# Kernel tuning notes

Hardware: AMD Instinct MI355X
Metric: run time of the kernel (lower is better)

Reference implementation:

```python
import jax, jax.numpy as jnp
import numpy as np

B, L, E, H = 4, 4096, 1024, 16
D = E // H  # head_dim = 64
EPS = 1e-4


def setup_inputs() -> dict:
    key = jax.random.key(0)
    k1, k2, k3 = jax.random.split(key, 3)
    x = jax.random.normal(k1, (B, L, E), dtype=jnp.float32)
    W_qkv = jax.random.normal(k2, (E, 3 * E), dtype=jnp.float32) * (1.0 / np.sqrt(E))
    b_qkv = jnp.zeros((3 * E,), dtype=jnp.float32)
    W_out = jax.random.normal(k3, (E, E), dtype=jnp.float32) * (1.0 / np.sqrt(E))
    b_out = jnp.zeros((E,), dtype=jnp.float32)
    return {"x": x, "W_qkv": W_qkv, "b_qkv": b_qkv, "W_out": W_out, "b_out": b_out}


def reference(x, W_qkv, b_qkv, W_out, b_out):
    Bb, Ll, Ee = x.shape
    qkv = x @ W_qkv + b_qkv                      # [B, L, 3E]
    q, k, v = jnp.split(qkv, 3, axis=-1)
    # [B, H, L, D]
    q = q.reshape(Bb, Ll, H, D).transpose(0, 2, 1, 3)
    k = k.reshape(Bb, Ll, H, D).transpose(0, 2, 1, 3)
    v = v.reshape(Bb, Ll, H, D).transpose(0, 2, 1, 3)

    positions = jnp.arange(Ll, dtype=jnp.float32).reshape(1, 1, Ll, 1)
    cos_w = jnp.cos(jnp.pi / 2 * positions / Ll)
    sin_w = jnp.sin(jnp.pi / 2 * positions / Ll)

    q_prime = jax.nn.relu(q)
    k_prime = jax.nn.relu(k)

    q_cos, q_sin = q_prime * cos_w, q_prime * sin_w
    k_cos, k_sin = k_prime * cos_w, k_prime * sin_w

    # O(L) linear attention: accumulate KV outer products per head
    kv_cos = jnp.einsum('bhld,bhle->bhde', k_cos, v)      # [B,H,D,D]
    kv_sin = jnp.einsum('bhld,bhle->bhde', k_sin, v)
    context = (jnp.einsum('bhld,bhde->bhle', q_cos, kv_cos)
               + jnp.einsum('bhld,bhde->bhle', q_sin, kv_sin))  # [B,H,L,D]

    k_cos_sum = k_cos.sum(axis=2)                          # [B,H,D]
    k_sin_sum = k_sin.sum(axis=2)
    norm = (jnp.einsum('bhld,bhd->bhl', q_cos, k_cos_sum)
            + jnp.einsum('bhld,bhd->bhl', q_sin, k_sin_sum))

    output = context / (norm[..., None] + EPS)
    output = output.transpose(0, 2, 1, 3).reshape(Bb, Ll, Ee)
    return output @ W_out + b_out
```

## Files before the change

kernel.cpp:

```cpp
#include <hip/hip_runtime.h>
#include <hip/hip_bf16.h>
#include <cstdint>
#include <cstddef>

#define BB 4
#define LL 4096
#define HH 16
#define M1 16384
#define E3 3072
#define EE 1024
#define ANGC 3.8349519697141029e-4f
#define EPSC 1e-4f

typedef __attribute__((ext_vector_type(8))) short bf16x8;
typedef __attribute__((ext_vector_type(4))) float f32x4;
typedef __attribute__((ext_vector_type(8))) unsigned short us8;

static __device__ __forceinline__ float bf2f(unsigned short u) {
  union { unsigned int i; float f; } a; a.i = ((unsigned int)u) << 16; return a.f;
}
static __device__ __forceinline__ unsigned short f2bf(float x) {
  union { float f; unsigned int i; } a; a.f = x;
  unsigned int r = a.i + 0x7FFFu + ((a.i >> 16) & 1u);
  return (unsigned short)(r >> 16);
}
static __device__ __forceinline__ void gload16(const void* g, void* l) {
  __builtin_amdgcn_global_load_lds((const __attribute__((address_space(1))) void*)g,
                                   (__attribute__((address_space(3))) void*)l, 16, 0, 0);
}

#define BAR()   asm volatile("s_barrier" ::: "memory")
#define VMC4()  asm volatile("s_waitcnt vmcnt(4)" ::: "memory")
#define VMC0()  asm volatile("s_waitcnt vmcnt(0)" ::: "memory")
#define PRIO1() __builtin_amdgcn_s_setprio(1)
#define PRIO0() __builtin_amdgcn_s_setprio(0)

__global__ __launch_bounds__(256) void k_cvt_bf16(const float* __restrict__ src,
                                                  unsigned short* __restrict__ dst, int n8) {
  int i = blockIdx.x * 256 + threadIdx.x;
  if (i >= n8) return;
  const float4* s = (const float4*)src + (size_t)i * 2;
  float4 a = s[0], b = s[1];
  us8 o;
  o[0]=f2bf(a.x); o[1]=f2bf(a.y); o[2]=f2bf(a.z); o[3]=f2bf(a.w);
  o[4]=f2bf(b.x); o[5]=f2bf(b.y); o[6]=f2bf(b.z); o[7]=f2bf(b.w);
  *(us8*)(dst + (size_t)i * 8) = o;
}

__global__ __launch_bounds__(256) void k_transpose_bf16(const float* __restrict__ src,
                                                        unsigned short* __restrict__ dst,
                                                        int R, int C) {
  __shared__ float tile[32][33];
  int c0 = blockIdx.x * 32, r0 = blockIdx.y * 32;
  int tx = threadIdx.x & 31, ty = threadIdx.x >> 5;
#pragma unroll
  for (int k = 0; k < 4; ++k)
    tile[ty + 8*k][tx] = src[(size_t)(r0 + ty + 8*k) * C + c0 + tx];
  __syncthreads();
#pragma unroll
  for (int k = 0; k < 4; ++k)
    dst[(size_t)(c0 + ty + 8*k) * R + r0 + tx] = f2bf(tile[tx][ty + 8*k]);
}


static __device__ __forceinline__ bf16x8 rdfrag(const char* base, int row, int ck) {
  return *(const bf16x8*)(base + row * 128 + (((ck) ^ ((row) & 7)) << 4));
}

static __device__ __forceinline__ void stage2h(const unsigned short* __restrict__ base,
                                               size_t off, size_t rowK64, char* ldst) {
  gload16(base + off, ldst);
  gload16(base + off + rowK64, ldst + 8192);
}

#define PH_FIRST(AbP, BbP, AR)                                                  \
  do {                                                                          \
    _Pragma("unroll")                                                           \
    for (int n = 0; n < 4; ++n) {                                               \
      const int br = wc * 64 + n * 16 + lr;                                     \
      bF[n][0] = rdfrag((BbP), br, lg);                                         \
      bF[n][1] = rdfrag((BbP), br, 4 + lg);                                     \
    }                                                                           \
    AR[0][0] = rdfrag((AbP), wr * 128 + lr, lg);                                \
    AR[0][1] = rdfrag((AbP), wr * 128 + lr, 4 + lg);                            \
    AR[1][0] = rdfrag((AbP), wr * 128 + 16 + lr, lg);                           \
    AR[1][1] = rdfrag((AbP), wr * 128 + 16 + lr, 4 + lg);                       \
  } while (0)

#define PH_A(AbP, mb, AR)                                                       \
  do {                                                                          \
    AR[0][0] = rdfrag((AbP), wr * 128 + (mb) * 16 + lr, lg);                    \
    AR[0][1] = rdfrag((AbP), wr * 128 + (mb) * 16 + lr, 4 + lg);                \
    AR[1][0] = rdfrag((AbP), wr * 128 + (mb) * 16 + 16 + lr, lg);               \
    AR[1][1] = rdfrag((AbP), wr * 128 + (mb) * 16 + 16 + lr, 4 + lg);           \
  } while (0)

#define MMA16(mb, AR)                                                           \
  do {                                                                          \
    _Pragma("unroll")                                                           \
    for (int kk = 0; kk < 2; ++kk) {                                            \
      _Pragma("unroll")                                                         \
      for (int n = 0; n < 4; ++n) {                                             \
        acc[(mb)][n] = __builtin_amdgcn_mfma_f32_16x16x32_bf16(                 \
            AR[0][kk], bF[n][kk], acc[(mb)][n], 0, 0, 0);                       \
        acc[(mb) + 1][n] = __builtin_amdgcn_mfma_f32_16x16x32_bf16(             \
            AR[1][kk], bF[n][kk], acc[(mb) + 1][n], 0, 0, 0);                   \
      }                                                                         \
    }                                                                           \
  } while (0)

template<int MODE>
__global__ __launch_bounds__(512, 2) void k_gemm256(const unsigned short* __restrict__ A,
                                                    const unsigned short* __restrict__ Bt,
                                                    const float* __restrict__ bias,
                                                    void* __restrict__ Cout,
                                                    int N, int K) {
  __shared__ __align__(16) unsigned short lds[4][16384];
  const int tid = threadIdx.x;
  const int wid = tid >> 6, lane = tid & 63;
  const int lr = lane & 15, lg = lane >> 4;
  const int wr = wid >> 2, wc = wid & 3;

  const int nx = gridDim.x;
  const int rawbid = blockIdx.y * nx + blockIdx.x;
  const int xcd = rawbid & 7, s = rawbid >> 3;
  const int g = s >> 5, r = s & 31;
  const int bm = (xcd * 8 + (r & 7)) * 256;
  const int bn = (g * 4 + (r >> 3)) * 256;

  char* LA0 = (char*)&lds[0][0];
  char* LB0 = (char*)&lds[1][0];
  char* LA1 = (char*)&lds[2][0];
  char* LB1 = (char*)&lds[3][0];

  f32x4 acc[8][4] = {};
  bf16x8 bF[4][2], aF[2][2], aG[2][2];

  const int rr = tid >> 3, cc = tid & 7;
  const size_t rowK64 = (size_t)64 * K, rowK128 = (size_t)128 * K;
  const size_t aoff = (size_t)(bm + rr) * K + ((cc ^ (rr & 7)) << 3);
  const size_t boff = (size_t)(bn + rr) * K + ((cc ^ (rr & 7)) << 3);
  char* const dst16 = (char*)0 + tid * 16;

#define STAGE_A(h, kt, L) stage2h(A,  aoff + (h) * rowK128 + (kt), rowK64, (L) + (h) * 16384 + tid * 16)
#define STAGE_B(h, kt, L) stage2h(Bt, boff + (h) * rowK128 + (kt), rowK64, (L) + (h) * 16384 + tid * 16)

  const int NT = K >> 6, NI = NT >> 1;

  STAGE_A(0, 0, LA0); STAGE_A(1, 0, LA0);
  STAGE_B(0, 0, LB0); STAGE_B(1, 0, LB0);
  STAGE_B(0, 64, LB1); STAGE_B(1, 64, LB1);
  VMC4();
  BAR();

  for (int it = 0; it < NI; ++it) {
    const int kt1 = (2*it + 1) << 6;
    const int kt2 = (2*it + 2) << 6;
    const int kt3 = (2*it + 3) << 6;
    const bool s2 = kt2 < K, s3 = kt3 < K;

    PH_FIRST(LA0, LB0, aF);
    STAGE_A(0, kt1, LA1);
    BAR(); PRIO1(); MMA16(0, aF); PRIO0();

    PH_A(LA0, 2, aG);
    STAGE_A(1, kt1, LA1);
    BAR(); PRIO1(); MMA16(2, aG); PRIO0();

    PH_A(LA0, 4, aF);
    if (s2) STAGE_B(0, kt2, LB0);
    BAR(); PRIO1(); MMA16(4, aF); PRIO0();

    PH_A(LA0, 6, aG);
    if (s2) STAGE_B(1, kt2, LB0);
    BAR(); PRIO1(); MMA16(6, aG); PRIO0();
    if (it == NI - 1) { VMC0(); } else { VMC4(); }
    BAR();

    PH_FIRST(LA1, LB1, aF);
    if (s2) STAGE_A(0, kt2, LA0);
    BAR(); PRIO1(); MMA16(0, aF); PRIO0();

    PH_A(LA1, 2, aG);
    if (s2) STAGE_A(1, kt2, LA0);
    BAR(); PRIO1(); MMA16(2, aG); PRIO0();

    PH_A(LA1, 4, aF);
    if (s3) STAGE_B(0, kt3, LB1);
    BAR(); PRIO1(); MMA16(4, aF); PRIO0();

    PH_A(LA1, 6, aG);
    if (s3) STAGE_B(1, kt3, LB1);
    BAR(); PRIO1(); MMA16(6, aG); PRIO0();
    VMC4();
    BAR();
  }
#undef STAGE_A
#undef STAGE_B

  {
    float* strip = (float*)((char*)&lds[0][0] + wid * 16384);
    float bias_v[4]; bool relu_v[4];
#pragma unroll
    for (int n = 0; n < 4; ++n) {
      int col = bn + wc*64 + n*16 + lr;
      bias_v[n] = bias[col];
      relu_v[n] = (MODE == 0) && (col < 2048);
    }
#pragma unroll
    for (int m = 0; m < 8; ++m) {
#pragma unroll
      for (int n = 0; n < 4; ++n)
#pragma unroll
        for (int j = 0; j < 4; ++j) {
          float v = acc[m][n][j] + bias_v[n];
          if (relu_v[n]) v = fmaxf(v, 0.0f);
          strip[(lg*4 + j)*68 + n*16 + lr] = v;
        }
#pragma unroll
      for (int itr = 0; itr < 4; ++itr) {
        int ch = itr*64 + lane;
        int row = ch >> 4, cg = ch & 15;
        float4 v = *(const float4*)(strip + row*68 + cg*4);
        size_t base = (size_t)(bm + wr*128 + m*16 + row) * N + bn + wc*64 + cg*4;
        if (MODE == 0) {
          ushort4 o;
          o.x = f2bf(v.x); o.y = f2bf(v.y); o.z = f2bf(v.z); o.w = f2bf(v.w);
          *(ushort4*)((unsigned short*)Cout + base) = o;
        } else {
          *(float4*)((float*)Cout + base) = v;
        }
      }
    }
  }
  (void)dst16;
}

__global__ __launch_bounds__(256) void k_stage2(const unsigned short* __restrict__ qkv,
                                                float* __restrict__ kvb,
                                                float* __restrict__ ksumb) {
  __shared__ __align__(16) unsigned short kcT[4096];
  __shared__ __align__(16) unsigned short ksT[4096];
  __shared__ __align__(16) unsigned short vT [4096];
  const int tid = threadIdx.x;
  const int head = blockIdx.y;
  const int b = head >> 4, h = head & 15;
  const int lane = tid & 63, wid = tid >> 6;
  const int lr = lane & 15, lg = lane >> 4;
  const int mt = wid >> 1, eh = wid & 1;
  const int lp = tid & 31;
  const int piece = tid >> 5;

  f32x4 acc[2][4] = {};
  float ksacc = 0.0f;
  const int mtk = tid >> 6, dk = tid & 63;
  const size_t qbase = (size_t)b * LL * E3;

  for (int sc = 0; sc < 4; ++sc) {
    const int lbase = blockIdx.x * 256 + sc * 64;
    __syncthreads();
    {
      const int l0 = 2 * lp;
      const int p0 = lbase + l0;
      float s0, c0, s1, c1;
      __sincosf((float)p0 * ANGC, &s0, &c0);
      __sincosf((float)(p0 + 1) * ANGC, &s1, &c1);
      const unsigned short* kp = qkv + qbase + (size_t)p0 * E3 + 1024 + h*64 + piece*8;
      us8 kr0 = *(const us8*)kp;
      us8 kr1 = *(const us8*)(kp + E3);
      us8 vr0 = *(const us8*)(kp + 1024);
      us8 vr1 = *(const us8*)(kp + 1024 + E3);
#pragma unroll
      for (int i = 0; i < 8; ++i) {
        int d = piece*8 + i;
        float ka = bf2f(kr0[i]), kb = bf2f(kr1[i]);
        unsigned int kcp = (unsigned int)f2bf(c0*ka) | ((unsigned int)f2bf(c1*kb) << 16);
        unsigned int ksp = (unsigned int)f2bf(s0*ka) | ((unsigned int)f2bf(s1*kb) << 16);
        unsigned int vp  = (unsigned int)vr0[i] | ((unsigned int)vr1[i] << 16);
        int off = d*128 + ((((l0 >> 3) ^ (d & 7))) << 4) + (l0 & 7) * 2;
        *(unsigned int*)((char*)kcT + off) = kcp;
        *(unsigned int*)((char*)ksT + off) = ksp;
        *(unsigned int*)((char*)vT  + off) = vp;
      }
    }
    __syncthreads();
    if (tid < 128) {
      const unsigned short* basep = mtk ? ksT : kcT;
      float sum = 0.0f;
#pragma unroll
      for (int cch = 0; cch < 8; ++cch) {
        us8 r = *(const us8*)((const char*)basep + dk*128 + ((cch ^ (dk & 7)) << 4));
#pragma unroll
        for (int i = 0; i < 8; ++i) sum += bf2f(r[i]);
      }
      ksacc += sum;
    }
    {
      const unsigned short* kT = mt ? ksT : kcT;
      bf16x8 af[2][2], bf[2][4];
#pragma unroll
      for (int kk = 0; kk < 2; ++kk) {
#pragma unroll
        for (int m = 0; m < 2; ++m) {
          int e = eh*32 + m*16 + lr;
          af[kk][m] = *(const bf16x8*)((const char*)vT + e*128 + ((((kk*4)+lg) ^ (e & 7)) << 4));
        }
#pragma unroll
        for (int n = 0; n < 4; ++n) {
          int d = n*16 + lr;
          bf[kk][n] = *(const bf16x8*)((const char*)kT + d*128 + ((((kk*4)+lg) ^ (d & 7)) << 4));
        }
      }
#pragma unroll
      for (int kk = 0; kk < 2; ++kk)
#pragma unroll
        for (int m = 0; m < 2; ++m)
#pragma unroll
          for (int n = 0; n < 4; ++n)
            acc[m][n] = __builtin_amdgcn_mfma_f32_16x16x32_bf16(af[kk][m], bf[kk][n], acc[m][n], 0, 0, 0);
    }
  }
  float* dst = kvb + (size_t)head * 8192 + mt * 4096;
#pragma unroll
  for (int m = 0; m < 2; ++m)
#pragma unroll
    for (int n = 0; n < 4; ++n)
#pragma unroll
      for (int j = 0; j < 4; ++j) {
        int e = eh*32 + m*16 + lg*4 + j;
        int d = n*16 + lr;
        atomicAdd(&dst[e*64 + d], acc[m][n][j]);
      }
  if (tid < 128) atomicAdd(&ksumb[head*128 + mtk*64 + dk], ksacc);
}

__global__ __launch_bounds__(256) void k_stage3(const unsigned short* __restrict__ qkv,
                                                const float* __restrict__ kvb,
                                                const float* __restrict__ ksumb,
                                                unsigned short* __restrict__ att) {
  __shared__ __align__(16) unsigned short Bl[144 * 64];
  const int tid = threadIdx.x;
  const int head = blockIdx.y;
  const int b = head >> 4, h = head & 15;
  const int l0 = blockIdx.x * 128;
  const int lane = tid & 63, w = tid >> 6;
  const int lr = lane & 15, lg = lane >> 4;

  {
    int c = tid >> 1, half = tid & 1;
    const float* src = kvb + (size_t)head * 8192 + (c >> 6) * 4096 + (c & 63) * 64 + half * 32;
    float fv[32];
#pragma unroll
    for (int q = 0; q < 8; ++q) *(float4*)(fv + q*4) = *(const float4*)(src + q*4);
#pragma unroll
    for (int q2 = 0; q2 < 4; ++q2) {
      us8 o;
#pragma unroll
      for (int i = 0; i < 8; ++i) o[i] = f2bf(fv[q2*8 + i]);
      int chunk = half*4 + q2;
      *(us8*)((char*)Bl + c*128 + ((chunk ^ (c & 7)) << 4)) = o;
    }
    if (tid < 16) {
      int cc = 128 + (tid >> 3), q = tid & 7;
      const float* s2 = ksumb + head*128 + (tid >> 3)*64 + q*8;
      us8 o;
#pragma unroll
      for (int i = 0; i < 8; ++i) o[i] = f2bf(s2[i]);
      *(us8*)((char*)Bl + cc*128 + ((q ^ (cc & 7)) << 4)) = o;
    } else if (tid < 128) {
      int idx = tid - 16;
      int cc = 130 + (idx >> 3), q = idx & 7;
      us8 o = {0,0,0,0,0,0,0,0};
      *(us8*)((char*)Bl + cc*128 + ((q ^ (cc & 7)) << 4)) = o;
    }
  }
  __syncthreads();

  f32x4 acc[2][9] = {};
  bf16x8 af[2][2];
  const size_t qrow0 = (size_t)(b * LL + l0 + w * 32);
#pragma unroll
  for (int kk = 0; kk < 2; ++kk)
#pragma unroll
    for (int m = 0; m < 2; ++m)
      af[m][kk] = *(const bf16x8*)(qkv + (qrow0 + m*16 + lr) * E3 + h*64 + kk*32 + lg*8);
#pragma unroll
  for (int kk = 0; kk < 2; ++kk)
#pragma unroll
    for (int n = 0; n < 9; ++n) {
      int cc = n*16 + lr;
      bf16x8 bb = *(const bf16x8*)((const char*)Bl + cc*128 + ((((kk*4)+lg) ^ (cc & 7)) << 4));
#pragma unroll
      for (int m = 0; m < 2; ++m)
        acc[m][n] = __builtin_amdgcn_mfma_f32_16x16x32_bf16(af[m][kk], bb, acc[m][n], 0, 0, 0);
    }

  __syncthreads();
  unsigned short* strip = (unsigned short*)Bl + w * 2048;
#pragma unroll
  for (int m = 0; m < 2; ++m)
#pragma unroll
    for (int j = 0; j < 4; ++j) {
      int rloc = m*16 + lg*4 + j;
      int pos = l0 + w*32 + rloc;
      float s_, c_;
      __sincosf((float)pos * ANGC, &s_, &c_);
      float nc = __shfl(acc[m][8][j], lane & 48, 64);
      float ns = __shfl(acc[m][8][j], (lane & 48) | 1, 64);
      float rn = 1.0f / (c_ * nc + s_ * ns + EPSC);
#pragma unroll
      for (int n = 0; n < 4; ++n) {
        float ctx = (c_ * acc[m][n][j] + s_ * acc[m][n+4][j]) * rn;
        strip[rloc*64 + n*16 + lr] = f2bf(ctx);
      }
    }
  __syncthreads();
#pragma unroll
  for (int p = 0; p < 4; ++p) {
    int ch = p*64 + lane;
    int row = ch >> 3, piece = ch & 7;
    us8 o = *(const us8*)(strip + row*64 + piece*8);
    *(us8*)(att + (size_t)(b*LL + l0 + w*32 + row) * EE + h*64 + piece*8) = o;
  }
}

extern "C" void kernel_launch(void* const* d_in, const int* in_sizes, int n_in,
                              void* d_out, int out_size, void* d_ws, size_t ws_size,
                              hipStream_t stream) {
  const float* x     = (const float*)d_in[0];
  const float* W_qkv = (const float*)d_in[1];
  const float* b_qkv = (const float*)d_in[2];
  const float* W_out = (const float*)d_in[3];
  const float* b_out = (const float*)d_in[4];

  char* w = (char*)d_ws;
  unsigned short* xb  = (unsigned short*)(w);
  unsigned short* qkv = (unsigned short*)(w + 33554432);
  unsigned short* WqT = (unsigned short*)(w + 134217728);
  unsigned short* WoT = (unsigned short*)(w + 140509184);
  float* kvb   = (float*)(w + 142606336);
  float* ksum  = (float*)(w + 144703488);
  unsigned short* att = xb;

  hipMemsetAsync(kvb, 0, 2097152 + 32768, stream);
  k_cvt_bf16<<<8192, 256, 0, stream>>>(x, xb, 2097152);
  k_transpose_bf16<<<dim3(96, 32), 256, 0, stream>>>(W_qkv, WqT, 1024, 3072);
  k_transpose_bf16<<<dim3(32, 32), 256, 0, stream>>>(W_out, WoT, 1024, 1024);
  k_gemm256<0><<<dim3(12, 64), 512, 0, stream>>>(xb, WqT, b_qkv, (void*)qkv, 3072, 1024);
  k_stage2<<<dim3(16, 64), 256, 0, stream>>>(qkv, kvb, ksum);
  k_stage3<<<dim3(32, 64), 256, 0, stream>>>(qkv, kvb, ksum, att);
  k_gemm256<1><<<dim3(4, 64), 512, 0, stream>>>(att, WoT, b_out, d_out, 1024, 1024);
}
```

Before: 237.1 us.

## Switch GEMM to 32x32x16 MFMA tiles and fuse prep kernels into one launch

The GEMM inner loop moves from 16x16x32 bf16 MFMA fragments to 32x32x16 MFMA, changing the register fragment layout, the LDS read pattern and the epilogue row mapping. The aim is fewer LDS fragment reads per FLOP and denser matrix-core issue. Launch bounds drop from 2 to 1 blocks per CU, which gives more registers for the larger accumulators but lowers occupancy. The conversion and two weight-transpose kernels are merged into a single launch to cut launch overhead.

```diff
diff --git a/kernel.cpp b/kernel.cpp
--- a/kernel.cpp
+++ b/kernel.cpp
@@ -14,6 +14,7 @@
 
 typedef __attribute__((ext_vector_type(8))) short bf16x8;
 typedef __attribute__((ext_vector_type(4))) float f32x4;
+typedef __attribute__((ext_vector_type(16))) float f32x16;
 typedef __attribute__((ext_vector_type(8))) unsigned short us8;
 
 static __device__ __forceinline__ float bf2f(unsigned short u) {
@@ -35,23 +36,11 @@
 #define PRIO1() __builtin_amdgcn_s_setprio(1)
 #define PRIO0() __builtin_amdgcn_s_setprio(0)
 
-__global__ __launch_bounds__(256) void k_cvt_bf16(const float* __restrict__ src,
-                                                  unsigned short* __restrict__ dst, int n8) {
-  int i = blockIdx.x * 256 + threadIdx.x;
-  if (i >= n8) return;
-  const float4* s = (const float4*)src + (size_t)i * 2;
-  float4 a = s[0], b = s[1];
-  us8 o;
-  o[0]=f2bf(a.x); o[1]=f2bf(a.y); o[2]=f2bf(a.z); o[3]=f2bf(a.w);
-  o[4]=f2bf(b.x); o[5]=f2bf(b.y); o[6]=f2bf(b.z); o[7]=f2bf(b.w);
-  *(us8*)(dst + (size_t)i * 8) = o;
-}
-
-__global__ __launch_bounds__(256) void k_transpose_bf16(const float* __restrict__ src,
-                                                        unsigned short* __restrict__ dst,
-                                                        int R, int C) {
-  __shared__ float tile[32][33];
-  int c0 = blockIdx.x * 32, r0 = blockIdx.y * 32;
+static __device__ __forceinline__ void transpose_body(const float* __restrict__ src,
+                                                      unsigned short* __restrict__ dst,
+                                                      int R, int C, int bx, int by,
+                                                      float (*tile)[33]) {
+  int c0 = bx * 32, r0 = by * 32;
   int tx = threadIdx.x & 31, ty = threadIdx.x >> 5;
 #pragma unroll
   for (int k = 0; k < 4; ++k)
@@ -60,6 +49,31 @@
 #pragma unroll
   for (int k = 0; k < 4; ++k)
     dst[(size_t)(c0 + ty + 8*k) * R + r0 + tx] = f2bf(tile[tx][ty + 8*k]);
+}
+
+__global__ __launch_bounds__(256) void k_prep(const float* __restrict__ x,
+                                              const float* __restrict__ Wq,
+                                              const float* __restrict__ Wo,
+                                              unsigned short* __restrict__ xb,
+                                              unsigned short* __restrict__ WqT,
+                                              unsigned short* __restrict__ WoT) {
+  __shared__ float tile[32][33];
+  const int bid = blockIdx.x;
+  if (bid < 8192) {
+    int i = bid * 256 + threadIdx.x;
+    const float4* s = (const float4*)x + (size_t)i * 2;
+    float4 a = s[0], b = s[1];
+    us8 o;
+    o[0]=f2bf(a.x); o[1]=f2bf(a.y); o[2]=f2bf(a.z); o[3]=f2bf(a.w);
+    o[4]=f2bf(b.x); o[5]=f2bf(b.y); o[6]=f2bf(b.z); o[7]=f2bf(b.w);
+    *(us8*)(xb + (size_t)i * 8) = o;
+  } else if (bid < 8192 + 3072) {
+    int r = bid - 8192;
+    transpose_body(Wq, WqT, 1024, 3072, r % 96, r / 96, tile);
+  } else {
+    int r = bid - 11264;
+    transpose_body(Wo, WoT, 1024, 1024, r % 32, r / 32, tile);
+  }
 }
 
 
@@ -73,44 +87,35 @@
   gload16(base + off + rowK64, ldst + 8192);
 }
 
-#define PH_FIRST(AbP, BbP, AR)                                                  \
+#define PH_B(BbP)                                                               \
   do {                                                                          \
     _Pragma("unroll")                                                           \
-    for (int n = 0; n < 4; ++n) {                                               \
-      const int br = wc * 64 + n * 16 + lr;                                     \
-      bF[n][0] = rdfrag((BbP), br, lg);                                         \
-      bF[n][1] = rdfrag((BbP), br, 4 + lg);                                     \
-    }                                                                           \
-    AR[0][0] = rdfrag((AbP), wr * 128 + lr, lg);                                \
-    AR[0][1] = rdfrag((AbP), wr * 128 + lr, 4 + lg);                            \
-    AR[1][0] = rdfrag((AbP), wr * 128 + 16 + lr, lg);                           \
-    AR[1][1] = rdfrag((AbP), wr * 128 + 16 + lr, 4 + lg);                       \
+    for (int nb = 0; nb < 2; ++nb)                                              \
+      _Pragma("unroll")                                                         \
+      for (int kk = 0; kk < 4; ++kk)                                            \
+        bK[nb][kk] = rdfrag((BbP), wc * 64 + nb * 32 + l31, kk * 2 + l5);       \
   } while (0)
 
-#define PH_A(AbP, mb, AR)                                                       \
-  do {                                                                          \
-    AR[0][0] = rdfrag((AbP), wr * 128 + (mb) * 16 + lr, lg);                    \
-    AR[0][1] = rdfrag((AbP), wr * 128 + (mb) * 16 + lr, 4 + lg);                \
-    AR[1][0] = rdfrag((AbP), wr * 128 + (mb) * 16 + 16 + lr, lg);               \
-    AR[1][1] = rdfrag((AbP), wr * 128 + (mb) * 16 + 16 + lr, 4 + lg);           \
-  } while (0)
-
-#define MMA16(mb, AR)                                                           \
+#define PH_A32(AbP, mb, AR)                                                     \
   do {                                                                          \
     _Pragma("unroll")                                                           \
-    for (int kk = 0; kk < 2; ++kk) {                                            \
-      _Pragma("unroll")                                                         \
-      for (int n = 0; n < 4; ++n) {                                             \
-        acc[(mb)][n] = __builtin_amdgcn_mfma_f32_16x16x32_bf16(                 \
-            AR[0][kk], bF[n][kk], acc[(mb)][n], 0, 0, 0);                       \
-        acc[(mb) + 1][n] = __builtin_amdgcn_mfma_f32_16x16x32_bf16(             \
-            AR[1][kk], bF[n][kk], acc[(mb) + 1][n], 0, 0, 0);                   \
-      }                                                                         \
+    for (int kk = 0; kk < 4; ++kk)                                              \
+      AR[kk] = rdfrag((AbP), wr * 128 + (mb) * 32 + l31, kk * 2 + l5);          \
+  } while (0)
+
+#define MMA8(mb, AR)                                                            \
+  do {                                                                          \
+    _Pragma("unroll")                                                           \
+    for (int kk = 0; kk < 4; ++kk) {                                            \
+      acc[(mb)][0] = __builtin_amdgcn_mfma_f32_32x32x16_bf16(                   \
+          AR[kk], bK[0][kk], acc[(mb)][0], 0, 0, 0);                            \
+      acc[(mb)][1] = __builtin_amdgcn_mfma_f32_32x32x16_bf16(                   \
+          AR[kk], bK[1][kk], acc[(mb)][1], 0, 0, 0);                            \
     }                                                                           \
   } while (0)
 
 template<int MODE>
-__global__ __launch_bounds__(512, 2) void k_gemm256(const unsigned short* __restrict__ A,
+__global__ __launch_bounds__(512, 1) void k_gemm256(const unsigned short* __restrict__ A,
                                                     const unsigned short* __restrict__ Bt,
                                                     const float* __restrict__ bias,
                                                     void* __restrict__ Cout,
@@ -118,7 +123,7 @@
   __shared__ __align__(16) unsigned short lds[4][16384];
   const int tid = threadIdx.x;
   const int wid = tid >> 6, lane = tid & 63;
-  const int lr = lane & 15, lg = lane >> 4;
+  const int l31 = lane & 31, l5 = lane >> 5;
   const int wr = wid >> 2, wc = wid & 3;
 
   const int nx = gridDim.x;
@@ -133,14 +138,13 @@
   char* LA1 = (char*)&lds[2][0];
   char* LB1 = (char*)&lds[3][0];
 
-  f32x4 acc[8][4] = {};
-  bf16x8 bF[4][2], aF[2][2], aG[2][2];
+  f32x16 acc[4][2] = {};
+  bf16x8 bK[2][4], aP[4], aQ[4];
 
   const int rr = tid >> 3, cc = tid & 7;
   const size_t rowK64 = (size_t)64 * K, rowK128 = (size_t)128 * K;
   const size_t aoff = (size_t)(bm + rr) * K + ((cc ^ (rr & 7)) << 3);
   const size_t boff = (size_t)(bn + rr) * K + ((cc ^ (rr & 7)) << 3);
-  char* const dst16 = (char*)0 + tid * 16;
 
 #define STAGE_A(h, kt, L) stage2h(A,  aoff + (h) * rowK128 + (kt), rowK64, (L) + (h) * 16384 + tid * 16)
 #define STAGE_B(h, kt, L) stage2h(Bt, boff + (h) * rowK128 + (kt), rowK64, (L) + (h) * 16384 + tid * 16)
@@ -159,39 +163,39 @@
     const int kt3 = (2*it + 3) << 6;
     const bool s2 = kt2 < K, s3 = kt3 < K;
 
-    PH_FIRST(LA0, LB0, aF);
+    PH_B(LB0); PH_A32(LA0, 0, aP);
     STAGE_A(0, kt1, LA1);
-    BAR(); PRIO1(); MMA16(0, aF); PRIO0();
-
-    PH_A(LA0, 2, aG);
+    BAR(); PRIO1(); MMA8(0, aP); PRIO0();
+
+    PH_A32(LA0, 1, aQ);
     STAGE_A(1, kt1, LA1);
-    BAR(); PRIO1(); MMA16(2, aG); PRIO0();
-
-    PH_A(LA0, 4, aF);
+    BAR(); PRIO1(); MMA8(1, aQ); PRIO0();
+
+    PH_A32(LA0, 2, aP);
     if (s2) STAGE_B(0, kt2, LB0);
-    BAR(); PRIO1(); MMA16(4, aF); PRIO0();
-
-    PH_A(LA0, 6, aG);
+    BAR(); PRIO1(); MMA8(2, aP); PRIO0();
+
+    PH_A32(LA0, 3, aQ);
     if (s2) STAGE_B(1, kt2, LB0);
-    BAR(); PRIO1(); MMA16(6, aG); PRIO0();
+    BAR(); PRIO1(); MMA8(3, aQ); PRIO0();
     if (it == NI - 1) { VMC0(); } else { VMC4(); }
     BAR();
 
-    PH_FIRST(LA1, LB1, aF);
+    PH_B(LB1); PH_A32(LA1, 0, aP);
     if (s2) STAGE_A(0, kt2, LA0);
-    BAR(); PRIO1(); MMA16(0, aF); PRIO0();
-
-    PH_A(LA1, 2, aG);
+    BAR(); PRIO1(); MMA8(0, aP); PRIO0();
+
+    PH_A32(LA1, 1, aQ);
     if (s2) STAGE_A(1, kt2, LA0);
-    BAR(); PRIO1(); MMA16(2, aG); PRIO0();
-
-    PH_A(LA1, 4, aF);
+    BAR(); PRIO1(); MMA8(1, aQ); PRIO0();
+
+    PH_A32(LA1, 2, aP);
     if (s3) STAGE_B(0, kt3, LB1);
-    BAR(); PRIO1(); MMA16(4, aF); PRIO0();
-
-    PH_A(LA1, 6, aG);
+    BAR(); PRIO1(); MMA8(2, aP); PRIO0();
+
+    PH_A32(LA1, 3, aQ);
     if (s3) STAGE_B(1, kt3, LB1);
-    BAR(); PRIO1(); MMA16(6, aG); PRIO0();
+    BAR(); PRIO1(); MMA8(3, aQ); PRIO0();
     VMC4();
     BAR();
   }
@@ -200,29 +204,30 @@
 
   {
     float* strip = (float*)((char*)&lds[0][0] + wid * 16384);
-    float bias_v[4]; bool relu_v[4];
-#pragma unroll
-    for (int n = 0; n < 4; ++n) {
-      int col = bn + wc*64 + n*16 + lr;
-      bias_v[n] = bias[col];
-      relu_v[n] = (MODE == 0) && (col < 2048);
-    }
-#pragma unroll
-    for (int m = 0; m < 8; ++m) {
-#pragma unroll
-      for (int n = 0; n < 4; ++n)
-#pragma unroll
-        for (int j = 0; j < 4; ++j) {
-          float v = acc[m][n][j] + bias_v[n];
-          if (relu_v[n]) v = fmaxf(v, 0.0f);
-          strip[(lg*4 + j)*68 + n*16 + lr] = v;
+    float bias_v[2]; bool relu_v[2];
+#pragma unroll
+    for (int nb = 0; nb < 2; ++nb) {
+      int col = bn + wc*64 + nb*32 + l31;
+      bias_v[nb] = bias[col];
+      relu_v[nb] = (MODE == 0) && (col < 2048);
+    }
+#pragma unroll
+    for (int mb = 0; mb < 4; ++mb) {
+#pragma unroll
+      for (int nb = 0; nb < 2; ++nb)
+#pragma unroll
+        for (int j = 0; j < 16; ++j) {
+          float v = acc[mb][nb][j] + bias_v[nb];
+          if (relu_v[nb]) v = fmaxf(v, 0.0f);
+          int row = (j & 3) + 8*(j >> 2) + 4*l5;
+          strip[row*68 + nb*32 + l31] = v;
         }
 #pragma unroll
-      for (int itr = 0; itr < 4; ++itr) {
+      for (int itr = 0; itr < 8; ++itr) {
         int ch = itr*64 + lane;
         int row = ch >> 4, cg = ch & 15;
         float4 v = *(const float4*)(strip + row*68 + cg*4);
-        size_t base = (size_t)(bm + wr*128 + m*16 + row) * N + bn + wc*64 + cg*4;
+        size_t base = (size_t)(bm + wr*128 + mb*32 + row) * N + bn + wc*64 + cg*4;
         if (MODE == 0) {
           ushort4 o;
           o.x = f2bf(v.x); o.y = f2bf(v.y); o.z = f2bf(v.z); o.w = f2bf(v.w);
@@ -233,7 +238,6 @@
       }
     }
   }
-  (void)dst16;
 }
 
 __global__ __launch_bounds__(256) void k_stage2(const unsigned short* __restrict__ qkv,
@@ -289,9 +293,9 @@
       float sum = 0.0f;
 #pragma unroll
       for (int cch = 0; cch < 8; ++cch) {
-        us8 r = *(const us8*)((const char*)basep + dk*128 + ((cch ^ (dk & 7)) << 4));
-#pragma unroll
-        for (int i = 0; i < 8; ++i) sum += bf2f(r[i]);
+        us8 r2 = *(const us8*)((const char*)basep + dk*128 + ((cch ^ (dk & 7)) << 4));
+#pragma unroll
+        for (int i = 0; i < 8; ++i) sum += bf2f(r2[i]);
       }
       ksacc += sum;
     }
@@ -443,9 +447,7 @@
   unsigned short* att = xb;
 
   hipMemsetAsync(kvb, 0, 2097152 + 32768, stream);
-  k_cvt_bf16<<<8192, 256, 0, stream>>>(x, xb, 2097152);
-  k_transpose_bf16<<<dim3(96, 32), 256, 0, stream>>>(W_qkv, WqT, 1024, 3072);
-  k_transpose_bf16<<<dim3(32, 32), 256, 0, stream>>>(W_out, WoT, 1024, 1024);
+  k_prep<<<12288, 256, 0, stream>>>(x, W_qkv, W_out, xb, WqT, WoT);
   k_gemm256<0><<<dim3(12, 64), 512, 0, stream>>>(xb, WqT, b_qkv, (void*)qkv, 3072, 1024);
   k_stage2<<<dim3(16, 64), 256, 0, stream>>>(qkv, kvb, ksum);
   k_stage3<<<dim3(32, 64), 256, 0, stream>>>(qkv, kvb, ksum, att);
```

New measurement: 236.7 us. Within noise of the previous version (-0.1%).
